# Kernel tuning notes

Measured on AMD Instinct MI355X. Metric: run time of the kernel, lower is better.

The kernel has to match this reference:

```python
import jax, jax.numpy as jnp
import numpy as np

WINDOW_SIZE = 2
SOFTMAX_TEMP = 0.01


def get_indices(batch_size, window_size):
    # For each window, match keypoints of frame j against dense map of frame j+1.
    kp_inds, dense_inds = [], []
    for i in range(batch_size):
        for j in range(window_size - 1):
            idx = i * window_size + j
            kp_inds.append(idx)
            dense_inds.append(idx + 1)
    return np.array(kp_inds), np.array(dense_inds)


def l2_normalize(x, axis):
    n = jnp.sqrt(jnp.sum(x * x, axis=axis, keepdims=True))
    return x / jnp.maximum(n, 1e-12)


def grid_sample_bilinear(img, grid_u, grid_v):
    """torch.nn.functional.grid_sample, mode='bilinear', padding='zeros', align_corners=False.
    img: (B,C,H,W); grid_u, grid_v: (B,N) normalized coords in [-1,1]. Returns (B,C,N)."""
    B, C, H, W = img.shape
    x = ((grid_u + 1.0) * W - 1.0) * 0.5  # pixel x
    y = ((grid_v + 1.0) * H - 1.0) * 0.5  # pixel y
    x0 = jnp.floor(x)
    y0 = jnp.floor(y)
    wx1 = x - x0
    wy1 = y - y0
    flat = img.reshape(B, C, H * W)

    def gather(xi, yi):
        valid = (xi >= 0) & (xi <= W - 1) & (yi >= 0) & (yi <= H - 1)
        xi_c = jnp.clip(xi, 0, W - 1).astype(jnp.int32)
        yi_c = jnp.clip(yi, 0, H - 1).astype(jnp.int32)
        idx = yi_c * W + xi_c  # (B,N)
        vals = jnp.take_along_axis(flat, idx[:, None, :], axis=2)  # (B,C,N)
        return vals * valid[:, None, :].astype(img.dtype)

    out = (gather(x0, y0) * ((1 - wx1) * (1 - wy1))[:, None, :]
           + gather(x0 + 1, y0) * (wx1 * (1 - wy1))[:, None, :]
           + gather(x0, y0 + 1) * ((1 - wx1) * wy1)[:, None, :]
           + gather(x0 + 1, y0 + 1) * (wx1 * wy1)[:, None, :])
    return out


def setup_inputs() -> dict:
    key = jax.random.key(0)
    k1, k2, k3, k4 = jax.random.split(key, 4)
    BW, C, N, H, W = 8, 128, 512, 256, 256
    return {
        "keypoint_scores": jax.random.uniform(k1, (BW, 1, N), dtype=jnp.float32),
        "keypoint_desc": jax.random.normal(k2, (BW, C, N), dtype=jnp.float32),
        "scores_dense": jax.random.uniform(k3, (BW, 1, H, W), dtype=jnp.float32),
        "desc_dense": jax.random.normal(k4, (BW, C, H, W), dtype=jnp.float32),
    }


def reference(keypoint_scores, keypoint_desc, scores_dense, desc_dense):
    BW, C, N = keypoint_desc.shape
    batch_size = BW // WINDOW_SIZE
    _, _, H, W = desc_dense.shape
    kp_inds, dense_inds = get_indices(batch_size, WINDOW_SIZE)

    src_desc = l2_normalize(keypoint_desc[kp_inds], axis=1)  # (B,C,N)
    B = src_desc.shape[0]
    tgt_desc_dense = desc_dense[dense_inds]  # (B,C,H,W)
    tgt_unrolled = l2_normalize(tgt_desc_dense.reshape(B, C, H * W), axis=1)

    # cosine similarity scores (B,N,H*W) -> temperature softmax over dense map
    match_vals = jnp.einsum('bcn,bcm->bnm', src_desc, tgt_unrolled)
    soft_match_vals = jax.nn.softmax(match_vals / SOFTMAX_TEMP, axis=2)

    # soft-argmax: expected (u,v) pixel coordinates
    v_coord, u_coord = jnp.meshgrid(jnp.arange(H), jnp.arange(W), indexing='ij')
    coords = jnp.stack([u_coord.reshape(-1), v_coord.reshape(-1)], axis=1).astype(jnp.float32)  # (HW,2)
    pseudo_coords = jnp.einsum('bnm,mk->bnk', soft_match_vals, coords)  # (B,N,2)

    u_norm = 2.0 * pseudo_coords[:, :, 0] / (W - 1) - 1.0
    v_norm = 2.0 * pseudo_coords[:, :, 1] / (H - 1) - 1.0

    tgt_scores_dense = scores_dense[dense_inds]
    pseudo_scores = grid_sample_bilinear(tgt_scores_dense, u_norm, v_norm)  # (B,1,N)
    pseudo_desc = grid_sample_bilinear(tgt_desc_dense, u_norm, v_norm)      # (B,C,N)

    desc_match_score = jnp.sum(src_desc * pseudo_desc, axis=1, keepdims=True) / float(C)
    src_scores = keypoint_scores[kp_inds]
    match_weights = 0.5 * (desc_match_score + 1.0) * src_scores * pseudo_scores
    return (pseudo_coords, match_weights, soft_match_vals)
```

## Files before the change

kernel.cpp:

```cpp
#include <hip/hip_runtime.h>


typedef short  v8s __attribute__((ext_vector_type(8)));
typedef unsigned short v8u __attribute__((ext_vector_type(8)));
typedef float  v4f __attribute__((ext_vector_type(4)));

#define EXP2_SCALE 144.269504088896f
#define WAITV(N) asm volatile("s_waitcnt vmcnt(" #N ")" ::: "memory")

static const size_t O_AHI  = 0;
static const size_t O_ALO  = O_AHI  + 262144ull*2;
static const size_t O_SRCN = O_ALO  + 262144ull*2;
static const size_t O_BHI  = O_SRCN + 262144ull*4;
static const size_t O_BLO  = O_BHI  + 33554432ull*2;
static const size_t O_PART = O_BLO  + 33554432ull*2;
static const size_t O_ROWS = O_PART + 2048ull*512*8;

static __device__ inline unsigned short f2bf(float x) {
    unsigned u = __float_as_uint(x);
    u = u + 0x7FFFu + ((u >> 16) & 1u);
    return (unsigned short)(u >> 16);
}
static __device__ inline float bf2f(unsigned short h) {
    return __uint_as_float(((unsigned)h) << 16);
}

__device__ __forceinline__ void gl_lds16(const void* g, void* l) {
    auto gp = (const __attribute__((address_space(1))) unsigned int*)(uintptr_t)g;
    auto lp = (__attribute__((address_space(3))) unsigned int*)(uintptr_t)l;
    __builtin_amdgcn_global_load_lds(gp, lp, 16, 0, 0);
}

__global__ void __launch_bounds__(256) k_prep_src(const float* __restrict__ kd,
                                                  float* __restrict__ srcN,
                                                  unsigned short* __restrict__ Ahi,
                                                  unsigned short* __restrict__ Alo) {
    int gw = blockIdx.x * 4 + (threadIdx.x >> 6);
    int l  = threadIdx.x & 63;
    int b  = gw >> 9, n = gw & 511;
    const float* base = kd + (size_t)(2 * b) * 128 * 512;
    float x0 = base[l * 512 + n];
    float x1 = base[(l + 64) * 512 + n];
    float ss = x0 * x0 + x1 * x1;
#pragma unroll
    for (int m = 1; m < 64; m <<= 1) ss += __shfl_xor(ss, m, 64);
    float inv = 1.0f / fmaxf(sqrtf(ss), 1e-12f);
    float xn0 = x0 * inv, xn1 = x1 * inv;
    int ob = gw * 128;
    srcN[ob + l] = xn0;  srcN[ob + l + 64] = xn1;
    unsigned short h0 = f2bf(xn0), h1 = f2bf(xn1);
    Ahi[ob + l] = h0;        Ahi[ob + l + 64] = h1;
    Alo[ob + l] = f2bf(xn0 - bf2f(h0));
    Alo[ob + l + 64] = f2bf(xn1 - bf2f(h1));
}

__global__ void __launch_bounds__(256) k_prep_tgt(const float* __restrict__ dd,
                                                  unsigned short* __restrict__ Bhi,
                                                  unsigned short* __restrict__ Blo) {
    int t = blockIdx.x * 128 + (threadIdx.x >> 1);
    int h = threadIdx.x & 1;
    int b = t >> 16;
    int p = t & 65535;
    const float* src = dd + (size_t)(2 * b + 1) * 128 * 65536 + (size_t)(h * 64) * 65536 + p;
    float v[64];
    float ss = 0.f;
#pragma unroll
    for (int c = 0; c < 64; ++c) { float x = src[(size_t)c * 65536]; v[c] = x; ss += x * x; }
    ss += __shfl_xor(ss, 1, 64);
    float inv = 1.0f / fmaxf(sqrtf(ss), 1e-12f);
    size_t ob = (size_t)t * 128 + h * 64;
#pragma unroll
    for (int c8 = 0; c8 < 8; ++c8) {
        v8u h8, l8;
#pragma unroll
        for (int j = 0; j < 8; ++j) {
            float xn = v[c8 * 8 + j] * inv;
            unsigned short hh = f2bf(xn);
            h8[j] = hh;
            l8[j] = f2bf(xn - bf2f(hh));
        }
        *(v8u*)(Bhi + ob + c8 * 8) = h8;
        *(v8u*)(Blo + ob + c8 * 8) = l8;
    }
}

template <int MODE>
__global__ void __launch_bounds__(256, 2) k_gemm(const unsigned short* __restrict__ Ahi,
                                                 const unsigned short* __restrict__ Alo,
                                                 const unsigned short* __restrict__ Bhi,
                                                 const unsigned short* __restrict__ Blo,
                                                 const float4* __restrict__ rows,
                                                 float* __restrict__ part,
                                                 float* __restrict__ out,
                                                 const float* __restrict__ ksc,
                                                 const float* __restrict__ sd,
                                                 const float* __restrict__ dd,
                                                 const float* __restrict__ srcN) {
    __shared__ v4f bstage4[2048];
    __shared__ float paux[MODE == 1 ? 8192 : 512];
    char* bstage = (char*)bstage4;
    constexpr int NSTEP = (MODE == 0) ? 2 : 4;

    const int tid = threadIdx.x;
    const int l = tid & 63, w = tid >> 6;
    const int wm = w & 1, wn = w >> 1;
    const int l15 = l & 15, l16 = l >> 4;
    const int mtg = blockIdx.x, ny = blockIdx.y, b = blockIdx.z;
    const int mt0 = mtg * 16;
    float* osm = out + 6144;

    v8s ahi[4][4], alo[4][4];
    {
        const size_t ar = ((size_t)(b * 512 + ny * 128 + wn * 64 + l15)) * 128 + l16 * 8;
#pragma unroll
        for (int nf = 0; nf < 4; ++nf)
#pragma unroll
            for (int ksl = 0; ksl < 4; ++ksl) {
                ahi[nf][ksl] = *(const v8s*)(Ahi + ar + nf * 2048 + ksl * 32);
                alo[nf][ksl] = *(const v8s*)(Alo + ar + nf * 2048 + ksl * 32);
            }
    }
    float invs[4];
    if (MODE == 1) {
#pragma unroll
        for (int nf = 0; nf < 4; ++nf)
            invs[nf] = rows[b * 512 + ny * 128 + wn * 64 + nf * 16 + l15].x;
    }
    asm volatile("s_waitcnt vmcnt(0)" ::: "memory");

    size_t pxrow = ((size_t)b * 65536 + (size_t)mt0 * 128) * 128;

#define STAGE(s, buf, prow)                                                         \
    {                                                                               \
        const unsigned short* src = (((s) < 2) ? Bhi : Blo) + (prow) + (((s) & 1) << 6); \
        char* dst = bstage + (buf) * 16384;                                         \
        _Pragma("unroll")                                                           \
        for (int i = 0; i < 4; ++i) {                                               \
            int sl = tid + i * 256;                                                 \
            int rl = sl >> 3, gg = sl & 7;                                          \
            gl_lds16(src + rl * 128 + ((gg ^ (rl & 7)) << 3), dst + (sl << 4));     \
        }                                                                           \
    }

    STAGE(0, 0, pxrow);

    for (int mt = 0; mt < 16; ++mt) {
        v4f acc[4][4];
#pragma unroll
        for (int mf = 0; mf < 4; ++mf)
#pragma unroll
            for (int nf = 0; nf < 4; ++nf) { v4f z = {0.f, 0.f, 0.f, 0.f}; acc[mf][nf] = z; }

#pragma unroll
        for (int s = 0; s < NSTEP; ++s) {
            if (s < NSTEP - 1)    STAGE(s + 1, (s + 1) & 1, pxrow)
            else if (mt < 15)     STAGE(0, 0, pxrow + 16384)

            if (s == 0) {
                if (mt == 0)          WAITV(4);
                else if (MODE == 1)   WAITV(20);
                else                  WAITV(5);
            } else if (s == NSTEP - 1 && mt == 15) {
                WAITV(0);
            } else {
                WAITV(4);
            }
            __builtin_amdgcn_s_barrier();
            __builtin_amdgcn_sched_barrier(0);

            const char* bb = bstage + (s & 1) * 16384;
#pragma unroll
            for (int k2 = 0; k2 < 2; ++k2) {
                const int ksl = ((s & 1) << 1) | k2;
                v8s pxf[4];
#pragma unroll
                for (int mf = 0; mf < 4; ++mf) {
                    int r = wm * 64 + mf * 16 + l15;
                    pxf[mf] = *(const v8s*)(bb + r * 128 + ((((k2 << 2) | l16) ^ (r & 7)) << 4));
                }
#pragma unroll
                for (int mf = 0; mf < 4; ++mf)
#pragma unroll
                    for (int nf = 0; nf < 4; ++nf) {
                        acc[mf][nf] = __builtin_amdgcn_mfma_f32_16x16x32_bf16(pxf[mf], ahi[nf][ksl], acc[mf][nf], 0, 0, 0);
                        if (MODE == 0 || s < 2)
                            acc[mf][nf] = __builtin_amdgcn_mfma_f32_16x16x32_bf16(pxf[mf], alo[nf][ksl], acc[mf][nf], 0, 0, 0);
                    }
            }
            __builtin_amdgcn_sched_barrier(0);
            __builtin_amdgcn_s_barrier();
        }

        if (MODE == 0) {
            float sS[4], sM[4];
#pragma unroll
            for (int nf = 0; nf < 4; ++nf) { sS[nf] = 0.f; sM[nf] = 0.f; }
#pragma unroll
            for (int mf = 0; mf < 4; ++mf) {
                int mloc = wm * 64 + mf * 16 + l16 * 4;
#pragma unroll
                for (int nf = 0; nf < 4; ++nf)
#pragma unroll
                    for (int r = 0; r < 4; ++r) {
                        float e = __builtin_amdgcn_exp2f(fmaf(acc[mf][nf][r], EXP2_SCALE, -EXP2_SCALE));
                        sS[nf] += e;
                        sM[nf] = fmaf(e, (float)(mloc + r), sM[nf]);
                    }
            }
#pragma unroll
            for (int nf = 0; nf < 4; ++nf) {
                sS[nf] += __shfl_xor(sS[nf], 16, 64); sS[nf] += __shfl_xor(sS[nf], 32, 64);
                sM[nf] += __shfl_xor(sM[nf], 16, 64); sM[nf] += __shfl_xor(sM[nf], 32, 64);
            }
            if (l < 16) {
#pragma unroll
                for (int nf = 0; nf < 4; ++nf) {
                    paux[((w * 4 + nf) * 16 + l15) * 2 + 0] = sS[nf];
                    paux[((w * 4 + nf) * 16 + l15) * 2 + 1] = sM[nf];
                }
            }
            asm volatile("s_waitcnt lgkmcnt(0)" ::: "memory");
            __builtin_amdgcn_s_barrier();
            int q = tid & 1, p15 = (tid >> 1) & 15, pnf = (tid >> 5) & 3, pwn = tid >> 7;
            float vs = paux[(((pwn * 2 + 0) * 4 + pnf) * 16 + p15) * 2 + q]
                     + paux[(((pwn * 2 + 1) * 4 + pnf) * 16 + p15) * 2 + q];
            int rowg = b * 512 + ny * 128 + pwn * 64 + pnf * 16 + p15;
            part[((size_t)rowg * 512 + (mt0 + mt)) * 2 + q] = vs;
            __builtin_amdgcn_s_barrier();
        } else {
            const size_t ocol = (size_t)(mt0 + mt) * 128;
            const int g = tid & 31, rh = tid >> 5;
#pragma unroll
            for (int half = 0; half < 2; ++half) {
                if (wn == half) {
#pragma unroll
                    for (int mf = 0; mf < 4; ++mf) {
                        int mq = wm * 16 + mf * 4 + l16;
#pragma unroll
                        for (int nf = 0; nf < 4; ++nf) {
                            int nl = nf * 16 + l15;
                            v4f pv;
#pragma unroll
                            for (int r = 0; r < 4; ++r)
                                pv[r] = __builtin_amdgcn_exp2f(fmaf(acc[mf][nf][r], EXP2_SCALE, -EXP2_SCALE)) * invs[nf];
                            *(v4f*)((char*)paux + nl * 512 + ((mq ^ (nl & 7)) << 4)) = pv;
                        }
                    }
                }
                asm volatile("s_waitcnt lgkmcnt(0)" ::: "memory");
                __builtin_amdgcn_s_barrier();
                size_t orow = (size_t)(b * 512 + ny * 128 + half * 64);
#pragma unroll
                for (int it = 0; it < 8; ++it) {
                    int r = it * 8 + rh;
                    v4f v = *(const v4f*)((const char*)paux + r * 512 + ((g ^ (r & 7)) << 4));
                    __builtin_nontemporal_store(v, (v4f*)(osm + (orow + r) * 65536 + ocol + g * 4));
                }
                __builtin_amdgcn_s_barrier();
            }
        }
        pxrow += 16384;
    }
#undef STAGE

    if (MODE == 1) {
        const int bidx = mtg + 32 * ny + 128 * b;
        const int r = bidx * 4 + w;
        const int rb = r >> 9;
        float4 rs = rows[r];
        float u = rs.y, v = rs.z;
        float un = 2.0f * u / 255.0f - 1.0f;
        float vn = 2.0f * v / 255.0f - 1.0f;
        float x = ((un + 1.0f) * 256.0f - 1.0f) * 0.5f;
        float y = ((vn + 1.0f) * 256.0f - 1.0f) * 0.5f;
        float x0f = floorf(x), y0f = floorf(y);
        int x0 = (int)x0f, y0 = (int)y0f;
        int x1 = x0 + 1, y1 = y0 + 1;
        float wx1 = x - x0f, wy1 = y - y0f;
        float wx0 = 1.0f - wx1, wy0 = 1.0f - wy1;
        float m00 = ((x0 >= 0) & (x0 <= 255) & (y0 >= 0) & (y0 <= 255)) ? 1.f : 0.f;
        float m10 = ((x1 >= 0) & (x1 <= 255) & (y0 >= 0) & (y0 <= 255)) ? 1.f : 0.f;
        float m01 = ((x0 >= 0) & (x0 <= 255) & (y1 >= 0) & (y1 <= 255)) ? 1.f : 0.f;
        float m11 = ((x1 >= 0) & (x1 <= 255) & (y1 >= 0) & (y1 <= 255)) ? 1.f : 0.f;
        int cx0 = min(max(x0, 0), 255), cx1 = min(max(x1, 0), 255);
        int cy0 = min(max(y0, 0), 255), cy1 = min(max(y1, 0), 255);
        int i00 = cy0 * 256 + cx0, i10 = cy0 * 256 + cx1;
        int i01 = cy1 * 256 + cx0, i11 = cy1 * 256 + cx1;
        float w00 = wx0 * wy0 * m00, w10 = wx1 * wy0 * m10;
        float w01 = wx0 * wy1 * m01, w11 = wx1 * wy1 * m11;

        const float* sdb = sd + (size_t)(2 * rb + 1) * 65536;
        float ps = w00 * sdb[i00] + w10 * sdb[i10] + w01 * sdb[i01] + w11 * sdb[i11];

        const float* ddb = dd + (size_t)(2 * rb + 1) * 128 * 65536;
        float dot = 0.f;
#pragma unroll
        for (int h2 = 0; h2 < 2; ++h2) {
            int c = l + h2 * 64;
            const float* dc = ddb + (size_t)c * 65536;
            float pd = w00 * dc[i00] + w10 * dc[i10] + w01 * dc[i01] + w11 * dc[i11];
            dot += srcN[r * 128 + c] * pd;
        }
#pragma unroll
        for (int m = 1; m < 64; m <<= 1) dot += __shfl_xor(dot, m, 64);
        if (l == 0) {
            float dms = dot / 128.0f;
            float sscore = ksc[(2 * rb) * 512 + (r & 511)];
            out[4096 + r] = 0.5f * (dms + 1.0f) * sscore * ps;
        }
    }
}

__global__ void __launch_bounds__(256) k_reduce(const float2* __restrict__ part,
                                                float4* __restrict__ rows,
                                                float* __restrict__ out) {
    int r = blockIdx.x * 4 + (threadIdx.x >> 6);
    int l = threadIdx.x & 63;
    float S = 0.f, Su = 0.f, Sv = 0.f;
#pragma unroll
    for (int i = 0; i < 8; ++i) {
        int mtv = l + i * 64;
        float2 p = part[(size_t)r * 512 + mtv];
        S += p.x;
        Su += (float)((mtv & 1) * 128) * p.x + p.y;
        Sv += (float)(mtv >> 1) * p.x;
    }
#pragma unroll
    for (int m = 1; m < 64; m <<= 1) {
        S += __shfl_xor(S, m, 64);
        Su += __shfl_xor(Su, m, 64);
        Sv += __shfl_xor(Sv, m, 64);
    }
    if (l == 0) {
        float invS = 1.0f / S;
        float u = Su * invS, v = Sv * invS;
        rows[r] = make_float4(invS, u, v, 0.f);
        out[r * 2] = u;
        out[r * 2 + 1] = v;
    }
}

extern "C" void kernel_launch(void* const* d_in, const int* in_sizes, int n_in,
                              void* d_out, int out_size, void* d_ws, size_t ws_size,
                              hipStream_t stream) {
    const float* ksc = (const float*)d_in[0];
    const float* kd  = (const float*)d_in[1];
    const float* sd  = (const float*)d_in[2];
    const float* dd  = (const float*)d_in[3];
    float* out = (float*)d_out;
    char* ws = (char*)d_ws;

    unsigned short* Ahi  = (unsigned short*)(ws + O_AHI);
    unsigned short* Alo  = (unsigned short*)(ws + O_ALO);
    float*          srcN = (float*)(ws + O_SRCN);
    unsigned short* Bhi  = (unsigned short*)(ws + O_BHI);
    unsigned short* Blo  = (unsigned short*)(ws + O_BLO);
    float*          part = (float*)(ws + O_PART);
    float4*         rows = (float4*)(ws + O_ROWS);

    k_prep_src<<<512, 256, 0, stream>>>(kd, srcN, Ahi, Alo);
    k_prep_tgt<<<2048, 256, 0, stream>>>(dd, Bhi, Blo);
    k_gemm<0><<<dim3(32, 4, 4), 256, 0, stream>>>(Ahi, Alo, Bhi, Blo, rows, part, out, ksc, sd, dd, srcN);
    k_reduce<<<512, 256, 0, stream>>>((const float2*)part, rows, out);
    k_gemm<1><<<dim3(32, 4, 4), 256, 0, stream>>>(Ahi, Alo, Bhi, Blo, rows, part, out, ksc, sd, dd, srcN);
}
```

Measured before the change: 423.9 us.

## Use 512-thread blocks with full-K staging and direct global softmax stores

The GEMM kernels now run 8 waves per block, each handling a 64x32 sub-tile, and stage the full 128-wide K slice per pixel tile into a 32 KB LDS buffer (double-buffered) instead of two half-K steps. The LDS-based cross-wave reduction in mode 0 is removed: each wave writes its partial sums straight to a wider partial buffer, and k_reduce adds the two halves. In mode 1 the LDS transpose for output is dropped in favour of direct nontemporal stores of softmax values. The aim is fewer barriers and LDS round trips, at the cost of more LDS per block, lower per-wave register reuse, and less coalesced output stores.

Measured after the change: 411.6 us. 1.03x faster.

```diff
diff --git a/kernel.cpp b/kernel.cpp
--- a/kernel.cpp
+++ b/kernel.cpp
@@ -7,6 +7,8 @@
 
 #define EXP2_SCALE 144.269504088896f
 #define WAITV(N) asm volatile("s_waitcnt vmcnt(" #N ")" ::: "memory")
+#define SBAR()   __builtin_amdgcn_s_barrier()
+#define SCHED()  __builtin_amdgcn_sched_barrier(0)
 
 static const size_t O_AHI  = 0;
 static const size_t O_ALO  = O_AHI  + 262144ull*2;
@@ -14,7 +16,7 @@
 static const size_t O_BHI  = O_SRCN + 262144ull*4;
 static const size_t O_BLO  = O_BHI  + 33554432ull*2;
 static const size_t O_PART = O_BLO  + 33554432ull*2;
-static const size_t O_ROWS = O_PART + 2048ull*512*8;
+static const size_t O_ROWS = O_PART + 2048ull*512*16;
 
 static __device__ inline unsigned short f2bf(float x) {
     unsigned u = __float_as_uint(x);
@@ -85,7 +87,7 @@
 }
 
 template <int MODE>
-__global__ void __launch_bounds__(256, 2) k_gemm(const unsigned short* __restrict__ Ahi,
+__global__ void __launch_bounds__(512, 2) k_gemm(const unsigned short* __restrict__ Ahi,
                                                  const unsigned short* __restrict__ Alo,
                                                  const unsigned short* __restrict__ Bhi,
                                                  const unsigned short* __restrict__ Blo,
@@ -96,110 +98,87 @@
                                                  const float* __restrict__ sd,
                                                  const float* __restrict__ dd,
                                                  const float* __restrict__ srcN) {
-    __shared__ v4f bstage4[2048];
-    __shared__ float paux[MODE == 1 ? 8192 : 512];
+    __shared__ v4f bstage4[4096];
     char* bstage = (char*)bstage4;
-    constexpr int NSTEP = (MODE == 0) ? 2 : 4;
 
     const int tid = threadIdx.x;
     const int l = tid & 63, w = tid >> 6;
-    const int wm = w & 1, wn = w >> 1;
+    const int wm = w >> 2, wn = w & 3;
     const int l15 = l & 15, l16 = l >> 4;
     const int mtg = blockIdx.x, ny = blockIdx.y, b = blockIdx.z;
     const int mt0 = mtg * 16;
     float* osm = out + 6144;
 
-    v8s ahi[4][4], alo[4][4];
+    v8s ahi[2][4], alo[2][4];
     {
-        const size_t ar = ((size_t)(b * 512 + ny * 128 + wn * 64 + l15)) * 128 + l16 * 8;
-#pragma unroll
-        for (int nf = 0; nf < 4; ++nf)
+        const size_t ar = ((size_t)(b * 512 + ny * 128 + wn * 32 + l15)) * 128 + l16 * 8;
+#pragma unroll
+        for (int nf = 0; nf < 2; ++nf)
 #pragma unroll
             for (int ksl = 0; ksl < 4; ++ksl) {
                 ahi[nf][ksl] = *(const v8s*)(Ahi + ar + nf * 2048 + ksl * 32);
                 alo[nf][ksl] = *(const v8s*)(Alo + ar + nf * 2048 + ksl * 32);
             }
     }
-    float invs[4];
+    float invs[2];
     if (MODE == 1) {
 #pragma unroll
-        for (int nf = 0; nf < 4; ++nf)
-            invs[nf] = rows[b * 512 + ny * 128 + wn * 64 + nf * 16 + l15].x;
-    }
-    asm volatile("s_waitcnt vmcnt(0)" ::: "memory");
+        for (int nf = 0; nf < 2; ++nf)
+            invs[nf] = rows[b * 512 + ny * 128 + wn * 32 + nf * 16 + l15].x;
+    }
+    WAITV(0);
 
     size_t pxrow = ((size_t)b * 65536 + (size_t)mt0 * 128) * 128;
 
-#define STAGE(s, buf, prow)                                                         \
+#define STAGEU(SRC, prow, bufidx)                                                   \
     {                                                                               \
-        const unsigned short* src = (((s) < 2) ? Bhi : Blo) + (prow) + (((s) & 1) << 6); \
-        char* dst = bstage + (buf) * 16384;                                         \
+        const unsigned short* src_ = (SRC) + (prow);                                \
+        char* dst_ = bstage + (bufidx) * 32768;                                     \
         _Pragma("unroll")                                                           \
         for (int i = 0; i < 4; ++i) {                                               \
-            int sl = tid + i * 256;                                                 \
-            int rl = sl >> 3, gg = sl & 7;                                          \
-            gl_lds16(src + rl * 128 + ((gg ^ (rl & 7)) << 3), dst + (sl << 4));     \
+            int sl = tid + i * 512;                                                 \
+            int rl = sl >> 4, gg = sl & 15;                                         \
+            gl_lds16(src_ + rl * 128 + ((gg ^ (rl & 15)) << 3), dst_ + (sl << 4));  \
         }                                                                           \
     }
 
-    STAGE(0, 0, pxrow);
-
-    for (int mt = 0; mt < 16; ++mt) {
-        v4f acc[4][4];
-#pragma unroll
-        for (int mf = 0; mf < 4; ++mf)
-#pragma unroll
-            for (int nf = 0; nf < 4; ++nf) { v4f z = {0.f, 0.f, 0.f, 0.f}; acc[mf][nf] = z; }
-
-#pragma unroll
-        for (int s = 0; s < NSTEP; ++s) {
-            if (s < NSTEP - 1)    STAGE(s + 1, (s + 1) & 1, pxrow)
-            else if (mt < 15)     STAGE(0, 0, pxrow + 16384)
-
-            if (s == 0) {
-                if (mt == 0)          WAITV(4);
-                else if (MODE == 1)   WAITV(20);
-                else                  WAITV(5);
-            } else if (s == NSTEP - 1 && mt == 15) {
-                WAITV(0);
-            } else {
-                WAITV(4);
-            }
-            __builtin_amdgcn_s_barrier();
-            __builtin_amdgcn_sched_barrier(0);
-
-            const char* bb = bstage + (s & 1) * 16384;
-#pragma unroll
-            for (int k2 = 0; k2 < 2; ++k2) {
-                const int ksl = ((s & 1) << 1) | k2;
+#define PXF(bufbase, mf_, ksl_)                                                     \
+    (*(const v8s*)((bufbase) + (wm * 64 + (mf_) * 16 + l15) * 256 +                 \
+                   ((((ksl_) * 4 + l16) ^ ((wm * 64 + (mf_) * 16 + l15) & 15)) << 4)))
+
+    v4f acc[4][2];
+
+    if (MODE == 0) {
+        STAGEU(Bhi, pxrow, 0);
+        for (int mt = 0; mt < 16; ++mt) {
+            if (mt < 15) STAGEU(Bhi, pxrow + 16384, (mt + 1) & 1);
+            if (mt == 0) WAITV(4); else if (mt == 15) WAITV(0); else WAITV(6);
+            SBAR(); SCHED();
+            const char* bb = bstage + (mt & 1) * 32768;
+#pragma unroll
+            for (int mf = 0; mf < 4; ++mf)
+#pragma unroll
+                for (int nf = 0; nf < 2; ++nf) { v4f z = {0.f,0.f,0.f,0.f}; acc[mf][nf] = z; }
+#pragma unroll
+            for (int ksl = 0; ksl < 4; ++ksl) {
                 v8s pxf[4];
 #pragma unroll
-                for (int mf = 0; mf < 4; ++mf) {
-                    int r = wm * 64 + mf * 16 + l15;
-                    pxf[mf] = *(const v8s*)(bb + r * 128 + ((((k2 << 2) | l16) ^ (r & 7)) << 4));
-                }
+                for (int mf = 0; mf < 4; ++mf) pxf[mf] = PXF(bb, mf, ksl);
 #pragma unroll
                 for (int mf = 0; mf < 4; ++mf)
 #pragma unroll
-                    for (int nf = 0; nf < 4; ++nf) {
+                    for (int nf = 0; nf < 2; ++nf) {
                         acc[mf][nf] = __builtin_amdgcn_mfma_f32_16x16x32_bf16(pxf[mf], ahi[nf][ksl], acc[mf][nf], 0, 0, 0);
-                        if (MODE == 0 || s < 2)
-                            acc[mf][nf] = __builtin_amdgcn_mfma_f32_16x16x32_bf16(pxf[mf], alo[nf][ksl], acc[mf][nf], 0, 0, 0);
+                        acc[mf][nf] = __builtin_amdgcn_mfma_f32_16x16x32_bf16(pxf[mf], alo[nf][ksl], acc[mf][nf], 0, 0, 0);
                     }
             }
-            __builtin_amdgcn_sched_barrier(0);
-            __builtin_amdgcn_s_barrier();
-        }
-
-        if (MODE == 0) {
-            float sS[4], sM[4];
-#pragma unroll
-            for (int nf = 0; nf < 4; ++nf) { sS[nf] = 0.f; sM[nf] = 0.f; }
+            SCHED(); SBAR();
+            float sS[2] = {0.f, 0.f}, sM[2] = {0.f, 0.f};
 #pragma unroll
             for (int mf = 0; mf < 4; ++mf) {
                 int mloc = wm * 64 + mf * 16 + l16 * 4;
 #pragma unroll
-                for (int nf = 0; nf < 4; ++nf)
+                for (int nf = 0; nf < 2; ++nf)
 #pragma unroll
                     for (int r = 0; r < 4; ++r) {
                         float e = __builtin_amdgcn_exp2f(fmaf(acc[mf][nf][r], EXP2_SCALE, -EXP2_SCALE));
@@ -208,110 +187,128 @@
                     }
             }
 #pragma unroll
-            for (int nf = 0; nf < 4; ++nf) {
+            for (int nf = 0; nf < 2; ++nf) {
                 sS[nf] += __shfl_xor(sS[nf], 16, 64); sS[nf] += __shfl_xor(sS[nf], 32, 64);
                 sM[nf] += __shfl_xor(sM[nf], 16, 64); sM[nf] += __shfl_xor(sM[nf], 32, 64);
             }
             if (l < 16) {
 #pragma unroll
-                for (int nf = 0; nf < 4; ++nf) {
-                    paux[((w * 4 + nf) * 16 + l15) * 2 + 0] = sS[nf];
-                    paux[((w * 4 + nf) * 16 + l15) * 2 + 1] = sM[nf];
+                for (int nf = 0; nf < 2; ++nf) {
+                    int row = b * 512 + ny * 128 + wn * 32 + nf * 16 + l15;
+                    *(float2*)(part + (((size_t)row * 512 + (mt0 + mt)) * 2 + wm) * 2)
+                        = make_float2(sS[nf], sM[nf]);
                 }
             }
-            asm volatile("s_waitcnt lgkmcnt(0)" ::: "memory");
-            __builtin_amdgcn_s_barrier();
-            int q = tid & 1, p15 = (tid >> 1) & 15, pnf = (tid >> 5) & 3, pwn = tid >> 7;
-            float vs = paux[(((pwn * 2 + 0) * 4 + pnf) * 16 + p15) * 2 + q]
-                     + paux[(((pwn * 2 + 1) * 4 + pnf) * 16 + p15) * 2 + q];
-            int rowg = b * 512 + ny * 128 + pwn * 64 + pnf * 16 + p15;
-            part[((size_t)rowg * 512 + (mt0 + mt)) * 2 + q] = vs;
-            __builtin_amdgcn_s_barrier();
-        } else {
-            const size_t ocol = (size_t)(mt0 + mt) * 128;
-            const int g = tid & 31, rh = tid >> 5;
-#pragma unroll
-            for (int half = 0; half < 2; ++half) {
-                if (wn == half) {
-#pragma unroll
-                    for (int mf = 0; mf < 4; ++mf) {
-                        int mq = wm * 16 + mf * 4 + l16;
-#pragma unroll
-                        for (int nf = 0; nf < 4; ++nf) {
-                            int nl = nf * 16 + l15;
-                            v4f pv;
-#pragma unroll
-                            for (int r = 0; r < 4; ++r)
-                                pv[r] = __builtin_amdgcn_exp2f(fmaf(acc[mf][nf][r], EXP2_SCALE, -EXP2_SCALE)) * invs[nf];
-                            *(v4f*)((char*)paux + nl * 512 + ((mq ^ (nl & 7)) << 4)) = pv;
-                        }
+            pxrow += 16384;
+        }
+    } else {
+        STAGEU(Bhi, pxrow, 0);
+        for (int mt = 0; mt < 16; ++mt) {
+            STAGEU(Blo, pxrow, 1);
+            if (mt == 0) WAITV(4); else WAITV(12);
+            SBAR(); SCHED();
+            const char* b0 = bstage;
+#pragma unroll
+            for (int mf = 0; mf < 4; ++mf)
+#pragma unroll
+                for (int nf = 0; nf < 2; ++nf) { v4f z = {0.f,0.f,0.f,0.f}; acc[mf][nf] = z; }
+#pragma unroll
+            for (int ksl = 0; ksl < 4; ++ksl) {
+                v8s pxf[4];
+#pragma unroll
+                for (int mf = 0; mf < 4; ++mf) pxf[mf] = PXF(b0, mf, ksl);
+#pragma unroll
+                for (int mf = 0; mf < 4; ++mf)
+#pragma unroll
+                    for (int nf = 0; nf < 2; ++nf) {
+                        acc[mf][nf] = __builtin_amdgcn_mfma_f32_16x16x32_bf16(pxf[mf], ahi[nf][ksl], acc[mf][nf], 0, 0, 0);
+                        acc[mf][nf] = __builtin_amdgcn_mfma_f32_16x16x32_bf16(pxf[mf], alo[nf][ksl], acc[mf][nf], 0, 0, 0);
                     }
+            }
+            SCHED(); SBAR();
+            if (mt < 15) STAGEU(Bhi, pxrow + 16384, 0);
+            if (mt == 15) WAITV(0); else WAITV(4);
+            SBAR(); SCHED();
+            const char* b1 = bstage + 32768;
+#pragma unroll
+            for (int ksl = 0; ksl < 4; ++ksl) {
+                v8s pxf[4];
+#pragma unroll
+                for (int mf = 0; mf < 4; ++mf) pxf[mf] = PXF(b1, mf, ksl);
+#pragma unroll
+                for (int mf = 0; mf < 4; ++mf)
+#pragma unroll
+                    for (int nf = 0; nf < 2; ++nf)
+                        acc[mf][nf] = __builtin_amdgcn_mfma_f32_16x16x32_bf16(pxf[mf], ahi[nf][ksl], acc[mf][nf], 0, 0, 0);
+            }
+            SCHED(); SBAR();
+            size_t mg0 = (size_t)(mt0 + mt) * 128 + wm * 64 + l16 * 4;
+#pragma unroll
+            for (int mf = 0; mf < 4; ++mf)
+#pragma unroll
+                for (int nf = 0; nf < 2; ++nf) {
+                    v4f pv;
+#pragma unroll
+                    for (int r = 0; r < 4; ++r)
+                        pv[r] = __builtin_amdgcn_exp2f(fmaf(acc[mf][nf][r], EXP2_SCALE, -EXP2_SCALE)) * invs[nf];
+                    size_t ng = (size_t)(b * 512 + ny * 128 + wn * 32 + nf * 16 + l15);
+                    __builtin_nontemporal_store(pv, (v4f*)(osm + ng * 65536 + mg0 + mf * 16));
                 }
-                asm volatile("s_waitcnt lgkmcnt(0)" ::: "memory");
-                __builtin_amdgcn_s_barrier();
-                size_t orow = (size_t)(b * 512 + ny * 128 + half * 64);
-#pragma unroll
-                for (int it = 0; it < 8; ++it) {
-                    int r = it * 8 + rh;
-                    v4f v = *(const v4f*)((const char*)paux + r * 512 + ((g ^ (r & 7)) << 4));
-                    __builtin_nontemporal_store(v, (v4f*)(osm + (orow + r) * 65536 + ocol + g * 4));
-                }
-                __builtin_amdgcn_s_barrier();
-            }
+            pxrow += 16384;
         }
-        pxrow += 16384;
-    }
-#undef STAGE
-
-    if (MODE == 1) {
-        const int bidx = mtg + 32 * ny + 128 * b;
-        const int r = bidx * 4 + w;
-        const int rb = r >> 9;
-        float4 rs = rows[r];
-        float u = rs.y, v = rs.z;
-        float un = 2.0f * u / 255.0f - 1.0f;
-        float vn = 2.0f * v / 255.0f - 1.0f;
-        float x = ((un + 1.0f) * 256.0f - 1.0f) * 0.5f;
-        float y = ((vn + 1.0f) * 256.0f - 1.0f) * 0.5f;
-        float x0f = floorf(x), y0f = floorf(y);
-        int x0 = (int)x0f, y0 = (int)y0f;
-        int x1 = x0 + 1, y1 = y0 + 1;
-        float wx1 = x - x0f, wy1 = y - y0f;
-        float wx0 = 1.0f - wx1, wy0 = 1.0f - wy1;
-        float m00 = ((x0 >= 0) & (x0 <= 255) & (y0 >= 0) & (y0 <= 255)) ? 1.f : 0.f;
-        float m10 = ((x1 >= 0) & (x1 <= 255) & (y0 >= 0) & (y0 <= 255)) ? 1.f : 0.f;
-        float m01 = ((x0 >= 0) & (x0 <= 255) & (y1 >= 0) & (y1 <= 255)) ? 1.f : 0.f;
-        float m11 = ((x1 >= 0) & (x1 <= 255) & (y1 >= 0) & (y1 <= 255)) ? 1.f : 0.f;
-        int cx0 = min(max(x0, 0), 255), cx1 = min(max(x1, 0), 255);
-        int cy0 = min(max(y0, 0), 255), cy1 = min(max(y1, 0), 255);
-        int i00 = cy0 * 256 + cx0, i10 = cy0 * 256 + cx1;
-        int i01 = cy1 * 256 + cx0, i11 = cy1 * 256 + cx1;
-        float w00 = wx0 * wy0 * m00, w10 = wx1 * wy0 * m10;
-        float w01 = wx0 * wy1 * m01, w11 = wx1 * wy1 * m11;
-
-        const float* sdb = sd + (size_t)(2 * rb + 1) * 65536;
-        float ps = w00 * sdb[i00] + w10 * sdb[i10] + w01 * sdb[i01] + w11 * sdb[i11];
-
-        const float* ddb = dd + (size_t)(2 * rb + 1) * 128 * 65536;
-        float dot = 0.f;
-#pragma unroll
-        for (int h2 = 0; h2 < 2; ++h2) {
-            int c = l + h2 * 64;
-            const float* dc = ddb + (size_t)c * 65536;
-            float pd = w00 * dc[i00] + w10 * dc[i10] + w01 * dc[i01] + w11 * dc[i11];
-            dot += srcN[r * 128 + c] * pd;
+
+        if (w < 4) {
+            const int bidx = mtg + 32 * ny + 128 * b;
+            const int r = bidx * 4 + w;
+            const int rb = r >> 9;
+            float4 rs = rows[r];
+            float u = rs.y, v = rs.z;
+            float un = 2.0f * u / 255.0f - 1.0f;
+            float vn = 2.0f * v / 255.0f - 1.0f;
+            float x = ((un + 1.0f) * 256.0f - 1.0f) * 0.5f;
+            float y = ((vn + 1.0f) * 256.0f - 1.0f) * 0.5f;
+            float x0f = floorf(x), y0f = floorf(y);
+            int x0 = (int)x0f, y0 = (int)y0f;
+            int x1 = x0 + 1, y1 = y0 + 1;
+            float wx1 = x - x0f, wy1 = y - y0f;
+            float wx0 = 1.0f - wx1, wy0 = 1.0f - wy1;
+            float m00 = ((x0 >= 0) & (x0 <= 255) & (y0 >= 0) & (y0 <= 255)) ? 1.f : 0.f;
+            float m10 = ((x1 >= 0) & (x1 <= 255) & (y0 >= 0) & (y0 <= 255)) ? 1.f : 0.f;
+            float m01 = ((x0 >= 0) & (x0 <= 255) & (y1 >= 0) & (y1 <= 255)) ? 1.f : 0.f;
+            float m11 = ((x1 >= 0) & (x1 <= 255) & (y1 >= 0) & (y1 <= 255)) ? 1.f : 0.f;
+            int cx0 = min(max(x0, 0), 255), cx1 = min(max(x1, 0), 255);
+            int cy0 = min(max(y0, 0), 255), cy1 = min(max(y1, 0), 255);
+            int i00 = cy0 * 256 + cx0, i10 = cy0 * 256 + cx1;
+            int i01 = cy1 * 256 + cx0, i11 = cy1 * 256 + cx1;
+            float w00 = wx0 * wy0 * m00, w10 = wx1 * wy0 * m10;
+            float w01 = wx0 * wy1 * m01, w11 = wx1 * wy1 * m11;
+
+            const float* sdb = sd + (size_t)(2 * rb + 1) * 65536;
+            float ps = w00 * sdb[i00] + w10 * sdb[i10] + w01 * sdb[i01] + w11 * sdb[i11];
+
+            const float* ddb = dd + (size_t)(2 * rb + 1) * 128 * 65536;
+            float dot = 0.f;
+#pragma unroll
+            for (int h2 = 0; h2 < 2; ++h2) {
+                int c = l + h2 * 64;
+                const float* dc = ddb + (size_t)c * 65536;
+                float pd = w00 * dc[i00] + w10 * dc[i10] + w01 * dc[i01] + w11 * dc[i11];
+                dot += srcN[r * 128 + c] * pd;
+            }
+#pragma unroll
+            for (int m = 1; m < 64; m <<= 1) dot += __shfl_xor(dot, m, 64);
+            if (l == 0) {
+                float dms = dot / 128.0f;
+                float sscore = ksc[(2 * rb) * 512 + (r & 511)];
+                out[4096 + r] = 0.5f * (dms + 1.0f) * sscore * ps;
+            }
         }
-#pragma unroll
-        for (int m = 1; m < 64; m <<= 1) dot += __shfl_xor(dot, m, 64);
-        if (l == 0) {
-            float dms = dot / 128.0f;
-            float sscore = ksc[(2 * rb) * 512 + (r & 511)];
-            out[4096 + r] = 0.5f * (dms + 1.0f) * sscore * ps;
-        }
-    }
-}
-
-__global__ void __launch_bounds__(256) k_reduce(const float2* __restrict__ part,
+    }
+#undef STAGEU
+#undef PXF
+}
+
+__global__ void __launch_bounds__(256) k_reduce(const float4* __restrict__ part,
                                                 float4* __restrict__ rows,
                                                 float* __restrict__ out) {
     int r = blockIdx.x * 4 + (threadIdx.x >> 6);
@@ -319,11 +316,13 @@
     float S = 0.f, Su = 0.f, Sv = 0.f;
 #pragma unroll
     for (int i = 0; i < 8; ++i) {
-        int mtv = l + i * 64;
-        float2 p = part[(size_t)r * 512 + mtv];
-        S += p.x;
-        Su += (float)((mtv & 1) * 128) * p.x + p.y;
-        Sv += (float)(mtv >> 1) * p.x;
+        int mt = l + i * 64;
+        float4 pp = part[(size_t)r * 512 + mt];
+        float Sp = pp.x + pp.z;
+        float Mp = pp.y + pp.w;
+        S += Sp;
+        Su += (float)((mt & 1) * 128) * Sp + Mp;
+        Sv += (float)(mt >> 1) * Sp;
     }
 #pragma unroll
     for (int m = 1; m < 64; m <<= 1) {
@@ -360,7 +359,7 @@
 
     k_prep_src<<<512, 256, 0, stream>>>(kd, srcN, Ahi, Alo);
     k_prep_tgt<<<2048, 256, 0, stream>>>(dd, Bhi, Blo);
-    k_gemm<0><<<dim3(32, 4, 4), 256, 0, stream>>>(Ahi, Alo, Bhi, Blo, rows, part, out, ksc, sd, dd, srcN);
-    k_reduce<<<512, 256, 0, stream>>>((const float2*)part, rows, out);
-    k_gemm<1><<<dim3(32, 4, 4), 256, 0, stream>>>(Ahi, Alo, Bhi, Blo, rows, part, out, ksc, sd, dd, srcN);
-}
+    k_gemm<0><<<dim3(32, 4, 4), 512, 0, stream>>>(Ahi, Alo, Bhi, Blo, rows, part, out, ksc, sd, dd, srcN);
+    k_reduce<<<512, 256, 0, stream>>>((const float4*)part, rows, out);
+    k_gemm<1><<<dim3(32, 4, 4), 512, 0, stream>>>(Ahi, Alo, Bhi, Blo, rows, part, out, ksc, sd, dd, srcN);
+}
```
